# Performance work log

Measured on AMD Instinct MI355X. Metric: run time of the kernel, lower is better.

The kernel has to match this reference:

```python
import jax, jax.numpy as jnp
import numpy as np

N_NODES = 50000
N_EDGES = 800000
D_IN = 128
D_OUT = 128
NUM_RELS = 100


def setup_inputs() -> dict:
    key = jax.random.key(0)
    k1, k2, k3, k4, k5, k6, k7 = jax.random.split(key, 7)
    h = jax.random.normal(k1, (N_NODES, D_IN), dtype=jnp.float32)
    W = jax.random.normal(k2, (D_IN, D_OUT), dtype=jnp.float32) * 0.05
    attn = jax.random.normal(k3, (2 * D_OUT,), dtype=jnp.float32) * 0.05
    rel_emb = jax.random.normal(k4, (NUM_RELS, 1), dtype=jnp.float32)
    src = jax.random.randint(k5, (N_EDGES,), 0, N_NODES, dtype=jnp.int32)
    dst = jax.random.randint(k6, (N_EDGES,), 0, N_NODES, dtype=jnp.int32)
    etype = jax.random.randint(k7, (N_EDGES,), 0, NUM_RELS, dtype=jnp.int32)
    return {"h": h, "W": W, "attn": attn, "rel_emb": rel_emb,
            "src": src, "dst": dst, "etype": etype}


def reference(h, W, attn, rel_emb, src, dst, etype):
    # h: [N, d_in], W: [d_in, d_out], attn: [2*d_out], rel_emb: [R, 1]
    # src/dst/etype: [E]
    N = h.shape[0]
    d = W.shape[1]
    # padding_idx=0 in nn.Embedding -> row 0 is zero
    rel_table = rel_emb.at[0].set(0.0)
    z = h @ W  # [N, d_out]
    # attn_fc([z_src, z_dst]) = z_src @ a_l + z_dst @ a_r (split the concat-linear)
    s_src = z @ attn[:d]  # [N]
    s_dst = z @ attn[d:]  # [N]
    e = jax.nn.leaky_relu(s_src[src] + s_dst[dst])  # [E], slope 0.01 as in torch
    # segment softmax over incoming edges of each dst node
    m = jax.ops.segment_max(e, dst, num_segments=N)  # [N]
    ex = jnp.exp(e - m[dst])  # [E]
    denom = jax.ops.segment_sum(ex, dst, num_segments=N)  # [N]
    alpha = ex / denom[dst]  # [E]
    coef = rel_table[etype, 0] * alpha  # [E]  (rel_alpha * alpha)
    # weighted sum of source messages per destination node
    out = jax.ops.segment_sum(coef[:, None] * z[src], dst, num_segments=N)  # [N, d_out]
    return out
```

## Files before the change

kernel.cpp:

```cpp
#include <hip/hip_runtime.h>

#define D 128
#define GROWS 64
#define CHUNK 4096

typedef __attribute__((ext_vector_type(8))) short short8;
typedef __attribute__((ext_vector_type(4))) float float4v;

__device__ __forceinline__ ushort f2bf(float x) {
    uint u = __float_as_uint(x);
    return (ushort)((u + 0x7FFFu + ((u >> 16) & 1u)) >> 16);
}
__device__ __forceinline__ float bf_lo(uint u) { return __uint_as_float(u << 16); }
__device__ __forceinline__ float bf_hi(uint u) { return __uint_as_float(u & 0xFFFF0000u); }

__global__ __launch_bounds__(256) void convW_kernel(
    const float* __restrict__ W, ushort* __restrict__ Wtg)
{
    int idx = blockIdx.x * 256 + threadIdx.x;
    int k = idx >> 7, n = idx & 127;
    Wtg[n * 128 + k] = f2bf(W[idx]);
}

__global__ __launch_bounds__(512) void gemm_mfma_kernel(
    const float* __restrict__ h, const ushort* __restrict__ Wtg,
    const float* __restrict__ attn,
    ushort* __restrict__ zb, float* __restrict__ s_src, float* __restrict__ s_dst,
    int N)
{
    __shared__ ushort ht[GROWS * 136];
    __shared__ float psum_s[GROWS][2];
    __shared__ float psum_d[GROWS][2];
    const int tid = threadIdx.x;
    const int base = blockIdx.x * GROWS;

#pragma unroll
    for (int it = 0; it < 4; ++it) {
        int idx = it * 512 + tid;
        int r = idx >> 5, c4 = (idx & 31) * 4;
        float4 v = make_float4(0.f, 0.f, 0.f, 0.f);
        if (base + r < N) v = *(const float4*)&h[(size_t)(base + r) * D + c4];
        ushort4 u = make_ushort4(f2bf(v.x), f2bf(v.y), f2bf(v.z), f2bf(v.w));
        *(ushort4*)&ht[r * 136 + c4] = u;
    }
    __syncthreads();

    const int lane = tid & 63;
    const int wave = tid >> 6;
    const int wr = wave >> 1;
    const int wc = wave & 1;
    const int col = lane & 15;
    const int quad = lane >> 4;
    const int wm = wr * 16;

    float4v acc[4];
#pragma unroll
    for (int nt = 0; nt < 4; ++nt) acc[nt] = (float4v)(0.f);

#pragma unroll 1
    for (int kc = 0; kc < 128; kc += 32) {
        short8 a = *(const short8*)&ht[(wm + col) * 136 + kc + quad * 8];
#pragma unroll
        for (int nt = 0; nt < 4; ++nt) {
            short8 b = *(const short8*)&Wtg[(wc * 64 + nt * 16 + col) * 128 + kc + quad * 8];
            acc[nt] = __builtin_amdgcn_mfma_f32_16x16x32_bf16(a, b, acc[nt], 0, 0, 0);
        }
    }
    __syncthreads();

    float ps[4] = {0.f, 0.f, 0.f, 0.f}, pd[4] = {0.f, 0.f, 0.f, 0.f};
#pragma unroll
    for (int nt = 0; nt < 4; ++nt) {
        float aL = attn[wc * 64 + nt * 16 + col];
        float aR = attn[D + wc * 64 + nt * 16 + col];
#pragma unroll
        for (int reg = 0; reg < 4; ++reg) {
            float v = acc[nt][reg];
            ps[reg] = fmaf(v, aL, ps[reg]);
            pd[reg] = fmaf(v, aR, pd[reg]);
            ht[(wm + quad * 4 + reg) * 136 + wc * 64 + nt * 16 + col] = f2bf(v);
        }
    }
#pragma unroll
    for (int reg = 0; reg < 4; ++reg) {
#pragma unroll
        for (int off = 1; off < 16; off <<= 1) {
            ps[reg] += __shfl_xor(ps[reg], off);
            pd[reg] += __shfl_xor(pd[reg], off);
        }
        if (col == 0) {
            int rl = wm + quad * 4 + reg;
            psum_s[rl][wc] = ps[reg];
            psum_d[rl][wc] = pd[reg];
        }
    }
    __syncthreads();

    if (tid < GROWS && base + tid < N) {
        s_src[base + tid] = psum_s[tid][0] + psum_s[tid][1];
        s_dst[base + tid] = psum_d[tid][0] + psum_d[tid][1];
    }

#pragma unroll
    for (int it = 0; it < 2; ++it) {
        int idx = it * 512 + tid;
        int r = idx >> 4, c8 = idx & 15;
        if (base + r < N)
            *(uint4*)&zb[(size_t)(base + r) * D + c8 * 8] = *(uint4*)&ht[r * 136 + c8 * 8];
    }
}


__global__ __launch_bounds__(256) void binA_kernel(
    const int* __restrict__ dst, int* __restrict__ histm, int nhi, int E)
{
    __shared__ int hist[256];
    const int tid = threadIdx.x;
    hist[tid] = 0;
    __syncthreads();
    const int base = blockIdx.x * CHUNK;
#pragma unroll
    for (int it = 0; it < CHUNK / 256; ++it) {
        int i = base + it * 256 + tid;
        if (i < E) atomicAdd(&hist[dst[i] >> 8], 1);
    }
    __syncthreads();
    if (tid < nhi) histm[blockIdx.x * nhi + tid] = hist[tid];
}

__global__ __launch_bounds__(64) void binB1_kernel(
    int* __restrict__ histm, int* __restrict__ colsum, int nhi, int nchunk)
{
    const int b = blockIdx.x;
    const int t = threadIdx.x;
    const int K = (nchunk + 63) / 64;
    int v[8];
    int s = 0;
#pragma unroll
    for (int j = 0; j < 8; ++j) {
        int c = t * K + j;
        v[j] = (j < K && c < nchunk) ? histm[c * nhi + b] : 0;
        s += v[j];
    }
    int incl = s;
#pragma unroll
    for (int off = 1; off < 64; off <<= 1) {
        int u = __shfl_up(incl, off);
        if (t >= off) incl += u;
    }
    int run = incl - s;
#pragma unroll
    for (int j = 0; j < 8; ++j) {
        int c = t * K + j;
        if (j < K && c < nchunk) { histm[c * nhi + b] = run; run += v[j]; }
    }
    if (t == 63) colsum[b] = incl;
}

__global__ __launch_bounds__(256) void binB2_kernel(
    const int* __restrict__ colsum, int* __restrict__ bin_base, int nhi, int E)
{
    __shared__ int sc[256];
    const int t = threadIdx.x;
    int total = (t < nhi) ? colsum[t] : 0;
    sc[t] = total;
    __syncthreads();
    for (int off = 1; off < 256; off <<= 1) {
        int u = (t >= off) ? sc[t - off] : 0;
        __syncthreads();
        sc[t] += u;
        __syncthreads();
    }
    if (t < nhi) bin_base[t] = sc[t] - total;
    if (t == nhi - 1) bin_base[nhi] = sc[t];
}

__global__ __launch_bounds__(256) void binC_kernel(
    const int* __restrict__ src, const int* __restrict__ dst,
    const int* __restrict__ etype, const int* __restrict__ histm,
    const int* __restrict__ bin_base, uint* __restrict__ binned, int nhi, int E)
{
    __shared__ int cursor[256];
    const int tid = threadIdx.x;
    if (tid < nhi) cursor[tid] = bin_base[tid] + histm[blockIdx.x * nhi + tid];
    __syncthreads();
    const int base = blockIdx.x * CHUNK;
#pragma unroll
    for (int it = 0; it < CHUNK / 256; ++it) {
        int i = base + it * 256 + tid;
        if (i < E) {
            int d = dst[i];
            int pos = atomicAdd(&cursor[d >> 8], 1);
            binned[pos] = (uint)src[i] | ((uint)etype[i] << 16) | ((uint)(d & 255) << 23);
        }
    }
}

__global__ __launch_bounds__(256) void binD_kernel(
    const uint* __restrict__ binned, const int* __restrict__ bin_base,
    int* __restrict__ offsets, uint* __restrict__ csr, int N, int E)
{
    __shared__ int hist[256];
    __shared__ int cursor[256];
    const int t = threadIdx.x;
    const int hi = blockIdx.x;
    const int bb = bin_base[hi];
    const int be = bin_base[hi + 1];
    hist[t] = 0;
    __syncthreads();
    for (int i = bb + t; i < be; i += 256)
        atomicAdd(&hist[(binned[i] >> 23) & 0xFF], 1);
    __syncthreads();
    int total = hist[t];
    cursor[t] = total;
    __syncthreads();
    for (int off = 1; off < 256; off <<= 1) {
        int u = (t >= off) ? cursor[t - off] : 0;
        __syncthreads();
        cursor[t] += u;
        __syncthreads();
    }
    int excl = cursor[t] - total;
    int node = hi * 256 + t;
    if (node < N) offsets[node] = bb + excl;
    if (node == N - 1 || (hi == gridDim.x - 1 && t == 255)) offsets[N] = E;
    __syncthreads();
    cursor[t] = bb + excl;
    __syncthreads();
    for (int i = bb + t; i < be; i += 256) {
        uint pk = binned[i];
        int pos = atomicAdd(&cursor[(pk >> 23) & 0xFF], 1);
        csr[pos] = pk;
    }
}

__global__ __launch_bounds__(256) void aggregate_kernel(
    const uint* __restrict__ zb32, const float* __restrict__ s_src,
    const float* __restrict__ s_dst, const int* __restrict__ offsets,
    const uint* __restrict__ csr_packed, const float* __restrict__ rel_emb,
    float* __restrict__ out, int N, int R)
{
    __shared__ float rel_l[128];
    const int tid = threadIdx.x;
    if (tid < R) rel_l[tid] = (tid == 0) ? 0.f : rel_emb[tid];
    __syncthreads();

    const int lane = tid & 63;
    const int half = lane & 31;
    const int hsel = lane >> 5;
    const int d = blockIdx.x * 4 + (tid >> 6);
    if (d >= N) return;

    const int start = offsets[d];
    const int end = offsets[d + 1];
    const float sdst = s_dst[d];

    float m = -INFINITY, l = 0.f;
    float4 acc = make_float4(0.f, 0.f, 0.f, 0.f);

    for (int base = start; base < end; base += 64) {
        const int idx = base + lane;
        const bool valid = idx < end;
        const uint packed = valid ? csr_packed[idx] : 0;
        const int srcv = (int)(packed & 0xFFFF);
        const int et = (int)((packed >> 16) & 0x7F);
        float ev = -INFINITY;
        if (valid) {
            float x = s_src[srcv] + sdst;
            ev = (x > 0.f) ? x : 0.01f * x;
        }
        float cm = ev;
#pragma unroll
        for (int off = 32; off; off >>= 1) cm = fmaxf(cm, __shfl_xor(cm, off));
        const float newm = fmaxf(m, cm);
        const float scale = __expf(m - newm);
        const float p = valid ? __expf(ev - newm) : 0.f;
        float ssum = p;
#pragma unroll
        for (int off = 32; off; off >>= 1) ssum += __shfl_xor(ssum, off);
        l = l * scale + ssum;
        acc.x *= scale; acc.y *= scale; acc.z *= scale; acc.w *= scale;
        m = newm;

        const float w = p * rel_l[et];
        const int nv = min(64, end - base);
        for (int j = 0; j < nv; j += 4) {
            const int e0 = j + hsel, e1 = j + 2 + hsel;
            const float w0 = __shfl(w, e0);
            const float w1 = __shfl(w, e1);
            const int s0 = __shfl(srcv, e0);
            const int s1 = __shfl(srcv, e1);
            const uint2 u0 = *(const uint2*)(zb32 + (size_t)s0 * 64 + half * 2);
            const uint2 u1 = *(const uint2*)(zb32 + (size_t)s1 * 64 + half * 2);
            acc.x = fmaf(w0, bf_lo(u0.x), acc.x);
            acc.y = fmaf(w0, bf_hi(u0.x), acc.y);
            acc.z = fmaf(w0, bf_lo(u0.y), acc.z);
            acc.w = fmaf(w0, bf_hi(u0.y), acc.w);
            acc.x = fmaf(w1, bf_lo(u1.x), acc.x);
            acc.y = fmaf(w1, bf_hi(u1.x), acc.y);
            acc.z = fmaf(w1, bf_lo(u1.y), acc.z);
            acc.w = fmaf(w1, bf_hi(u1.y), acc.w);
        }
    }

    acc.x += __shfl_xor(acc.x, 32);
    acc.y += __shfl_xor(acc.y, 32);
    acc.z += __shfl_xor(acc.z, 32);
    acc.w += __shfl_xor(acc.w, 32);

    const float inv = (l > 0.f) ? 1.0f / l : 0.f;
    if (lane < 32) {
        float4 res = make_float4(acc.x * inv, acc.y * inv, acc.z * inv, acc.w * inv);
        *(float4*)(out + (size_t)d * D + 4 * half) = res;
    }
}

extern "C" void kernel_launch(void* const* d_in, const int* in_sizes, int n_in,
                              void* d_out, int out_size, void* d_ws, size_t ws_size,
                              hipStream_t stream)
{
    const float* h    = (const float*)d_in[0];
    const float* W    = (const float*)d_in[1];
    const float* attn = (const float*)d_in[2];
    const float* rel  = (const float*)d_in[3];
    const int*   src  = (const int*)d_in[4];
    const int*   dst  = (const int*)d_in[5];
    const int*   et   = (const int*)d_in[6];
    float* out = (float*)d_out;

    const int N = in_sizes[0] / D;
    const int E = in_sizes[4];
    const int R = in_sizes[3];

    char* p = (char*)d_ws;
    auto alloc = [&](size_t bytes) {
        char* q = p;
        p += (bytes + 255) & ~(size_t)255;
        return q;
    };
    const int nhi    = (N + 255) / 256;
    const int nchunk = (E + CHUNK - 1) / CHUNK;

    ushort* zb      = (ushort*)alloc((size_t)N * D * sizeof(ushort));
    ushort* Wtg     = (ushort*)alloc((size_t)D * D * sizeof(ushort));
    float* ssrc     = (float*)alloc((size_t)N * sizeof(float));
    float* sdst     = (float*)alloc((size_t)N * sizeof(float));
    int*   offsets  = (int*)alloc((size_t)(N + 1) * sizeof(int));
    uint*  binned   = (uint*)alloc((size_t)E * sizeof(uint));
    uint*  csr      = (uint*)alloc((size_t)E * sizeof(uint));
    int*   histm    = (int*)alloc((size_t)nchunk * nhi * sizeof(int));
    int*   colsum   = (int*)alloc((size_t)nhi * sizeof(int));
    int*   bin_base = (int*)alloc((size_t)(nhi + 1) * sizeof(int));

    const int gblocks = (N + GROWS - 1) / GROWS;

    convW_kernel<<<64, 256, 0, stream>>>(W, Wtg);
    gemm_mfma_kernel<<<gblocks, 512, 0, stream>>>(h, Wtg, attn, zb, ssrc, sdst, N);
    binA_kernel<<<nchunk, 256, 0, stream>>>(dst, histm, nhi, E);
    binB1_kernel<<<nhi, 64, 0, stream>>>(histm, colsum, nhi, nchunk);
    binB2_kernel<<<1, 256, 0, stream>>>(colsum, bin_base, nhi, E);
    binC_kernel<<<nchunk, 256, 0, stream>>>(src, dst, et, histm, bin_base, binned, nhi, E);
    binD_kernel<<<nhi, 256, 0, stream>>>(binned, bin_base, offsets, csr, N, E);
    aggregate_kernel<<<(N + 3) / 4, 256, 0, stream>>>((const uint*)zb, ssrc, sdst,
                                                      offsets, csr, rel, out, N, R);
}
```

Before: 179.4 us.

## Fuse five CSR binning kernels into one cooperative kernel with grid syncs

```diff
diff --git a/kernel.cpp b/kernel.cpp
--- a/kernel.cpp
+++ b/kernel.cpp
@@ -1,8 +1,11 @@
 #include <hip/hip_runtime.h>
+#include <hip/hip_cooperative_groups.h>
+
+namespace cg = cooperative_groups;
 
 #define D 128
 #define GROWS 64
-#define CHUNK 4096
+#define SCHUNKS 256
 
 typedef __attribute__((ext_vector_type(8))) short short8;
 typedef __attribute__((ext_vector_type(4))) float float4v;
@@ -110,127 +113,103 @@
     }
 }
 
-
-__global__ __launch_bounds__(256) void binA_kernel(
-    const int* __restrict__ dst, int* __restrict__ histm, int nhi, int E)
-{
-    __shared__ int hist[256];
+__global__ __launch_bounds__(256) void coop_sort_kernel(
+    const int* __restrict__ src, const int* __restrict__ dst,
+    const int* __restrict__ etype,
+    int* __restrict__ histm,
+    int* __restrict__ colsum, int* __restrict__ bin_base,
+    uint* __restrict__ binned, int* __restrict__ offsets, uint* __restrict__ csr,
+    int nhi, int N, int E)
+{
+    cg::grid_group grid = cg::this_grid();
+    __shared__ int sA[256];
+    __shared__ int sB[256];
     const int tid = threadIdx.x;
-    hist[tid] = 0;
-    __syncthreads();
-    const int base = blockIdx.x * CHUNK;
-#pragma unroll
-    for (int it = 0; it < CHUNK / 256; ++it) {
-        int i = base + it * 256 + tid;
-        if (i < E) atomicAdd(&hist[dst[i] >> 8], 1);
-    }
-    __syncthreads();
-    if (tid < nhi) histm[blockIdx.x * nhi + tid] = hist[tid];
-}
-
-__global__ __launch_bounds__(64) void binB1_kernel(
-    int* __restrict__ histm, int* __restrict__ colsum, int nhi, int nchunk)
-{
-    const int b = blockIdx.x;
-    const int t = threadIdx.x;
-    const int K = (nchunk + 63) / 64;
-    int v[8];
-    int s = 0;
-#pragma unroll
-    for (int j = 0; j < 8; ++j) {
-        int c = t * K + j;
-        v[j] = (j < K && c < nchunk) ? histm[c * nhi + b] : 0;
-        s += v[j];
-    }
-    int incl = s;
-#pragma unroll
-    for (int off = 1; off < 64; off <<= 1) {
-        int u = __shfl_up(incl, off);
-        if (t >= off) incl += u;
-    }
-    int run = incl - s;
-#pragma unroll
-    for (int j = 0; j < 8; ++j) {
-        int c = t * K + j;
-        if (j < K && c < nchunk) { histm[c * nhi + b] = run; run += v[j]; }
-    }
-    if (t == 63) colsum[b] = incl;
-}
-
-__global__ __launch_bounds__(256) void binB2_kernel(
-    const int* __restrict__ colsum, int* __restrict__ bin_base, int nhi, int E)
-{
-    __shared__ int sc[256];
-    const int t = threadIdx.x;
-    int total = (t < nhi) ? colsum[t] : 0;
-    sc[t] = total;
-    __syncthreads();
-    for (int off = 1; off < 256; off <<= 1) {
-        int u = (t >= off) ? sc[t - off] : 0;
-        __syncthreads();
-        sc[t] += u;
-        __syncthreads();
-    }
-    if (t < nhi) bin_base[t] = sc[t] - total;
-    if (t == nhi - 1) bin_base[nhi] = sc[t];
-}
-
-__global__ __launch_bounds__(256) void binC_kernel(
-    const int* __restrict__ src, const int* __restrict__ dst,
-    const int* __restrict__ etype, const int* __restrict__ histm,
-    const int* __restrict__ bin_base, uint* __restrict__ binned, int nhi, int E)
-{
-    __shared__ int cursor[256];
-    const int tid = threadIdx.x;
-    if (tid < nhi) cursor[tid] = bin_base[tid] + histm[blockIdx.x * nhi + tid];
-    __syncthreads();
-    const int base = blockIdx.x * CHUNK;
-#pragma unroll
-    for (int it = 0; it < CHUNK / 256; ++it) {
-        int i = base + it * 256 + tid;
-        if (i < E) {
-            int d = dst[i];
-            int pos = atomicAdd(&cursor[d >> 8], 1);
-            binned[pos] = (uint)src[i] | ((uint)etype[i] << 16) | ((uint)(d & 255) << 23);
-        }
-    }
-}
-
-__global__ __launch_bounds__(256) void binD_kernel(
-    const uint* __restrict__ binned, const int* __restrict__ bin_base,
-    int* __restrict__ offsets, uint* __restrict__ csr, int N, int E)
-{
-    __shared__ int hist[256];
-    __shared__ int cursor[256];
-    const int t = threadIdx.x;
-    const int hi = blockIdx.x;
-    const int bb = bin_base[hi];
-    const int be = bin_base[hi + 1];
-    hist[t] = 0;
-    __syncthreads();
-    for (int i = bb + t; i < be; i += 256)
-        atomicAdd(&hist[(binned[i] >> 23) & 0xFF], 1);
-    __syncthreads();
-    int total = hist[t];
-    cursor[t] = total;
-    __syncthreads();
-    for (int off = 1; off < 256; off <<= 1) {
-        int u = (t >= off) ? cursor[t - off] : 0;
-        __syncthreads();
-        cursor[t] += u;
-        __syncthreads();
-    }
-    int excl = cursor[t] - total;
-    int node = hi * 256 + t;
-    if (node < N) offsets[node] = bb + excl;
-    if (node == N - 1 || (hi == gridDim.x - 1 && t == 255)) offsets[N] = E;
-    __syncthreads();
-    cursor[t] = bb + excl;
-    __syncthreads();
-    for (int i = bb + t; i < be; i += 256) {
-        uint pk = binned[i];
-        int pos = atomicAdd(&cursor[(pk >> 23) & 0xFF], 1);
-        csr[pos] = pk;
+    const int blk = blockIdx.x;
+    const int cpb = (E + SCHUNKS - 1) / SCHUNKS;
+    const int cstart = blk * cpb;
+    const int cend = min(cstart + cpb, E);
+
+    sA[tid] = 0;
+    __syncthreads();
+    for (int i = cstart + tid; i < cend; i += 256)
+        atomicAdd(&sA[dst[i] >> 8], 1);
+    __syncthreads();
+    if (tid < nhi) histm[blk * nhi + tid] = sA[tid];
+
+    grid.sync();
+
+    if (blk < nhi) {
+        int v = histm[tid * nhi + blk];
+        sB[tid] = v;
+        __syncthreads();
+        for (int off = 1; off < 256; off <<= 1) {
+            int u = (tid >= off) ? sB[tid - off] : 0;
+            __syncthreads();
+            sB[tid] += u;
+            __syncthreads();
+        }
+        histm[tid * nhi + blk] = sB[tid] - v;
+        if (tid == 255) colsum[blk] = sB[255];
+    }
+
+    grid.sync();
+
+    if (blk == 0) {
+        int total = (tid < nhi) ? colsum[tid] : 0;
+        sB[tid] = total;
+        __syncthreads();
+        for (int off = 1; off < 256; off <<= 1) {
+            int u = (tid >= off) ? sB[tid - off] : 0;
+            __syncthreads();
+            sB[tid] += u;
+            __syncthreads();
+        }
+        if (tid < nhi) bin_base[tid] = sB[tid] - total;
+        if (tid == nhi - 1) bin_base[nhi] = sB[tid];
+    }
+
+    grid.sync();
+
+    if (tid < nhi) sB[tid] = bin_base[tid] + histm[blk * nhi + tid];
+    __syncthreads();
+    for (int i = cstart + tid; i < cend; i += 256) {
+        int d = dst[i];
+        int pos = atomicAdd(&sB[d >> 8], 1);
+        binned[pos] = (uint)src[i] | ((uint)etype[i] << 16) | ((uint)(d & 255) << 23);
+    }
+
+    grid.sync();
+
+    if (blk < nhi) {
+        const int bb = bin_base[blk];
+        const int be = bin_base[blk + 1];
+        sA[tid] = 0;
+        __syncthreads();
+        for (int i = bb + tid; i < be; i += 256)
+            atomicAdd(&sA[(binned[i] >> 23) & 0xFF], 1);
+        __syncthreads();
+        int total = sA[tid];
+        sB[tid] = total;
+        __syncthreads();
+        for (int off = 1; off < 256; off <<= 1) {
+            int u = (tid >= off) ? sB[tid - off] : 0;
+            __syncthreads();
+            sB[tid] += u;
+            __syncthreads();
+        }
+        int excl = sB[tid] - total;
+        int node = blk * 256 + tid;
+        if (node < N) offsets[node] = bb + excl;
+        if (node == N - 1) offsets[N] = E;
+        __syncthreads();
+        sB[tid] = bb + excl;
+        __syncthreads();
+        for (int i = bb + tid; i < be; i += 256) {
+            uint pk = binned[i];
+            int pos = atomicAdd(&sB[(pk >> 23) & 0xFF], 1);
+            csr[pos] = pk;
+        }
     }
 }
 
@@ -328,9 +307,9 @@
     const int*   et   = (const int*)d_in[6];
     float* out = (float*)d_out;
 
-    const int N = in_sizes[0] / D;
-    const int E = in_sizes[4];
-    const int R = in_sizes[3];
+    int N = in_sizes[0] / D;
+    int E = in_sizes[4];
+    int R = in_sizes[3];
 
     char* p = (char*)d_ws;
     auto alloc = [&](size_t bytes) {
@@ -338,8 +317,7 @@
         p += (bytes + 255) & ~(size_t)255;
         return q;
     };
-    const int nhi    = (N + 255) / 256;
-    const int nchunk = (E + CHUNK - 1) / CHUNK;
+    int nhi = (N + 255) / 256;
 
     ushort* zb      = (ushort*)alloc((size_t)N * D * sizeof(ushort));
     ushort* Wtg     = (ushort*)alloc((size_t)D * D * sizeof(ushort));
@@ -348,7 +326,7 @@
     int*   offsets  = (int*)alloc((size_t)(N + 1) * sizeof(int));
     uint*  binned   = (uint*)alloc((size_t)E * sizeof(uint));
     uint*  csr      = (uint*)alloc((size_t)E * sizeof(uint));
-    int*   histm    = (int*)alloc((size_t)nchunk * nhi * sizeof(int));
+    int*   histm    = (int*)alloc((size_t)SCHUNKS * nhi * sizeof(int));
     int*   colsum   = (int*)alloc((size_t)nhi * sizeof(int));
     int*   bin_base = (int*)alloc((size_t)(nhi + 1) * sizeof(int));
 
@@ -356,11 +334,17 @@
 
     convW_kernel<<<64, 256, 0, stream>>>(W, Wtg);
     gemm_mfma_kernel<<<gblocks, 512, 0, stream>>>(h, Wtg, attn, zb, ssrc, sdst, N);
-    binA_kernel<<<nchunk, 256, 0, stream>>>(dst, histm, nhi, E);
-    binB1_kernel<<<nhi, 64, 0, stream>>>(histm, colsum, nhi, nchunk);
-    binB2_kernel<<<1, 256, 0, stream>>>(colsum, bin_base, nhi, E);
-    binC_kernel<<<nchunk, 256, 0, stream>>>(src, dst, et, histm, bin_base, binned, nhi, E);
-    binD_kernel<<<nhi, 256, 0, stream>>>(binned, bin_base, offsets, csr, N, E);
+
+    const int* src_a = src; const int* dst_a = dst; const int* et_a = et;
+    void* sort_args[] = {
+        (void*)&src_a, (void*)&dst_a, (void*)&et_a,
+        (void*)&histm, (void*)&colsum, (void*)&bin_base,
+        (void*)&binned, (void*)&offsets, (void*)&csr,
+        (void*)&nhi, (void*)&N, (void*)&E
+    };
+    hipLaunchCooperativeKernel((void*)coop_sort_kernel, dim3(SCHUNKS), dim3(256),
+                               sort_args, 0, stream);
+
     aggregate_kernel<<<(N + 3) / 4, 256, 0, stream>>>((const uint*)zb, ssrc, sdst,
                                                       offsets, csr, rel, out, N, R);
 }
```

Result: slower. 310.3 us (+73.0%).

## Fuse dst histogram into GEMM, fold bin-base scan into binning kernels

Applied to the files above, without the earlier changes.

```diff
diff --git a/kernel.cpp b/kernel.cpp
--- a/kernel.cpp
+++ b/kernel.cpp
@@ -2,7 +2,6 @@
 
 #define D 128
 #define GROWS 64
-#define CHUNK 4096
 
 typedef __attribute__((ext_vector_type(8))) short short8;
 typedef __attribute__((ext_vector_type(4))) float float4v;
@@ -24,13 +23,14 @@
 
 __global__ __launch_bounds__(512) void gemm_mfma_kernel(
     const float* __restrict__ h, const ushort* __restrict__ Wtg,
-    const float* __restrict__ attn,
+    const float* __restrict__ attn, const int* __restrict__ dst,
     ushort* __restrict__ zb, float* __restrict__ s_src, float* __restrict__ s_dst,
-    int N)
+    int* __restrict__ histm, int nhi, int N, int E, int nblocks)
 {
     __shared__ ushort ht[GROWS * 136];
     __shared__ float psum_s[GROWS][2];
     __shared__ float psum_d[GROWS][2];
+    __shared__ int histA[256];
     const int tid = threadIdx.x;
     const int base = blockIdx.x * GROWS;
 
@@ -43,6 +43,7 @@
         ushort4 u = make_ushort4(f2bf(v.x), f2bf(v.y), f2bf(v.z), f2bf(v.w));
         *(ushort4*)&ht[r * 136 + c4] = u;
     }
+    if (tid < 256) histA[tid] = 0;
     __syncthreads();
 
     const int lane = tid & 63;
@@ -108,24 +109,14 @@
         if (base + r < N)
             *(uint4*)&zb[(size_t)(base + r) * D + c8 * 8] = *(uint4*)&ht[r * 136 + c8 * 8];
     }
-}
-
-
-__global__ __launch_bounds__(256) void binA_kernel(
-    const int* __restrict__ dst, int* __restrict__ histm, int nhi, int E)
-{
-    __shared__ int hist[256];
-    const int tid = threadIdx.x;
-    hist[tid] = 0;
-    __syncthreads();
-    const int base = blockIdx.x * CHUNK;
-#pragma unroll
-    for (int it = 0; it < CHUNK / 256; ++it) {
-        int i = base + it * 256 + tid;
-        if (i < E) atomicAdd(&hist[dst[i] >> 8], 1);
-    }
-    __syncthreads();
-    if (tid < nhi) histm[blockIdx.x * nhi + tid] = hist[tid];
+
+    const int cpb = (E + nblocks - 1) / nblocks;
+    const int cs = blockIdx.x * cpb;
+    const int ce = min(cs + cpb, E);
+    for (int i = cs + tid; i < ce; i += 512)
+        atomicAdd(&histA[dst[i] >> 8], 1);
+    __syncthreads();
+    if (tid < nhi) histm[blockIdx.x * nhi + tid] = histA[tid];
 }
 
 __global__ __launch_bounds__(64) void binB1_kernel(
@@ -134,10 +125,10 @@
     const int b = blockIdx.x;
     const int t = threadIdx.x;
     const int K = (nchunk + 63) / 64;
-    int v[8];
+    int v[16];
     int s = 0;
 #pragma unroll
-    for (int j = 0; j < 8; ++j) {
+    for (int j = 0; j < 16; ++j) {
         int c = t * K + j;
         v[j] = (j < K && c < nchunk) ? histm[c * nhi + b] : 0;
         s += v[j];
@@ -150,86 +141,87 @@
     }
     int run = incl - s;
 #pragma unroll
-    for (int j = 0; j < 8; ++j) {
+    for (int j = 0; j < 16; ++j) {
         int c = t * K + j;
         if (j < K && c < nchunk) { histm[c * nhi + b] = run; run += v[j]; }
     }
     if (t == 63) colsum[b] = incl;
-}
-
-__global__ __launch_bounds__(256) void binB2_kernel(
-    const int* __restrict__ colsum, int* __restrict__ bin_base, int nhi, int E)
-{
-    __shared__ int sc[256];
-    const int t = threadIdx.x;
-    int total = (t < nhi) ? colsum[t] : 0;
-    sc[t] = total;
-    __syncthreads();
-    for (int off = 1; off < 256; off <<= 1) {
-        int u = (t >= off) ? sc[t - off] : 0;
-        __syncthreads();
-        sc[t] += u;
-        __syncthreads();
-    }
-    if (t < nhi) bin_base[t] = sc[t] - total;
-    if (t == nhi - 1) bin_base[nhi] = sc[t];
 }
 
 __global__ __launch_bounds__(256) void binC_kernel(
     const int* __restrict__ src, const int* __restrict__ dst,
     const int* __restrict__ etype, const int* __restrict__ histm,
-    const int* __restrict__ bin_base, uint* __restrict__ binned, int nhi, int E)
-{
-    __shared__ int cursor[256];
+    const int* __restrict__ colsum, uint* __restrict__ binned,
+    int nhi, int E, int nchunk)
+{
+    __shared__ int sc[256];
+    __shared__ int cur[256];
     const int tid = threadIdx.x;
-    if (tid < nhi) cursor[tid] = bin_base[tid] + histm[blockIdx.x * nhi + tid];
-    __syncthreads();
-    const int base = blockIdx.x * CHUNK;
-#pragma unroll
-    for (int it = 0; it < CHUNK / 256; ++it) {
-        int i = base + it * 256 + tid;
-        if (i < E) {
-            int d = dst[i];
-            int pos = atomicAdd(&cursor[d >> 8], 1);
-            binned[pos] = (uint)src[i] | ((uint)etype[i] << 16) | ((uint)(d & 255) << 23);
-        }
+    int tot = (tid < nhi) ? colsum[tid] : 0;
+    sc[tid] = tot;
+    __syncthreads();
+    for (int off = 1; off < 256; off <<= 1) {
+        int u = (tid >= off) ? sc[tid - off] : 0;
+        __syncthreads();
+        sc[tid] += u;
+        __syncthreads();
+    }
+    if (tid < nhi) cur[tid] = (sc[tid] - tot) + histm[blockIdx.x * nhi + tid];
+    __syncthreads();
+    const int cpb = (E + nchunk - 1) / nchunk;
+    const int cs = blockIdx.x * cpb;
+    const int ce = min(cs + cpb, E);
+    for (int i = cs + tid; i < ce; i += 256) {
+        int d = dst[i];
+        int pos = atomicAdd(&cur[d >> 8], 1);
+        binned[pos] = (uint)src[i] | ((uint)etype[i] << 16) | ((uint)(d & 255) << 23);
     }
 }
 
 __global__ __launch_bounds__(256) void binD_kernel(
-    const uint* __restrict__ binned, const int* __restrict__ bin_base,
-    int* __restrict__ offsets, uint* __restrict__ csr, int N, int E)
-{
+    const uint* __restrict__ binned, const int* __restrict__ colsum,
+    int* __restrict__ offsets, uint* __restrict__ csr, int nhi, int N, int E)
+{
+    __shared__ int sc[256];
     __shared__ int hist[256];
-    __shared__ int cursor[256];
+    __shared__ int cur[256];
     const int t = threadIdx.x;
     const int hi = blockIdx.x;
-    const int bb = bin_base[hi];
-    const int be = bin_base[hi + 1];
+    int tot = (t < nhi) ? colsum[t] : 0;
+    sc[t] = tot;
+    __syncthreads();
+    for (int off = 1; off < 256; off <<= 1) {
+        int u = (t >= off) ? sc[t - off] : 0;
+        __syncthreads();
+        sc[t] += u;
+        __syncthreads();
+    }
+    const int bb = (hi == 0) ? 0 : sc[hi - 1];
+    const int be = sc[hi];
     hist[t] = 0;
     __syncthreads();
     for (int i = bb + t; i < be; i += 256)
         atomicAdd(&hist[(binned[i] >> 23) & 0xFF], 1);
     __syncthreads();
     int total = hist[t];
-    cursor[t] = total;
+    cur[t] = total;
     __syncthreads();
     for (int off = 1; off < 256; off <<= 1) {
-        int u = (t >= off) ? cursor[t - off] : 0;
-        __syncthreads();
-        cursor[t] += u;
-        __syncthreads();
-    }
-    int excl = cursor[t] - total;
+        int u = (t >= off) ? cur[t - off] : 0;
+        __syncthreads();
+        cur[t] += u;
+        __syncthreads();
+    }
+    int excl = cur[t] - total;
     int node = hi * 256 + t;
     if (node < N) offsets[node] = bb + excl;
-    if (node == N - 1 || (hi == gridDim.x - 1 && t == 255)) offsets[N] = E;
-    __syncthreads();
-    cursor[t] = bb + excl;
+    if (node == N - 1) offsets[N] = E;
+    __syncthreads();
+    cur[t] = bb + excl;
     __syncthreads();
     for (int i = bb + t; i < be; i += 256) {
         uint pk = binned[i];
-        int pos = atomicAdd(&cursor[(pk >> 23) & 0xFF], 1);
+        int pos = atomicAdd(&cur[(pk >> 23) & 0xFF], 1);
         csr[pos] = pk;
     }
 }
@@ -284,14 +276,16 @@
 
         const float w = p * rel_l[et];
         const int nv = min(64, end - base);
-        for (int j = 0; j < nv; j += 4) {
-            const int e0 = j + hsel, e1 = j + 2 + hsel;
-            const float w0 = __shfl(w, e0);
-            const float w1 = __shfl(w, e1);
-            const int s0 = __shfl(srcv, e0);
-            const int s1 = __shfl(srcv, e1);
+        for (int j = 0; j < nv; j += 8) {
+            const int e0 = j + hsel, e1 = j + 2 + hsel, e2 = j + 4 + hsel, e3 = j + 6 + hsel;
+            const float w0 = __shfl(w, e0), w1 = __shfl(w, e1);
+            const float w2 = __shfl(w, e2), w3 = __shfl(w, e3);
+            const int s0 = __shfl(srcv, e0), s1 = __shfl(srcv, e1);
+            const int s2 = __shfl(srcv, e2), s3 = __shfl(srcv, e3);
             const uint2 u0 = *(const uint2*)(zb32 + (size_t)s0 * 64 + half * 2);
             const uint2 u1 = *(const uint2*)(zb32 + (size_t)s1 * 64 + half * 2);
+            const uint2 u2 = *(const uint2*)(zb32 + (size_t)s2 * 64 + half * 2);
+            const uint2 u3 = *(const uint2*)(zb32 + (size_t)s3 * 64 + half * 2);
             acc.x = fmaf(w0, bf_lo(u0.x), acc.x);
             acc.y = fmaf(w0, bf_hi(u0.x), acc.y);
             acc.z = fmaf(w0, bf_lo(u0.y), acc.z);
@@ -300,6 +294,14 @@
             acc.y = fmaf(w1, bf_hi(u1.x), acc.y);
             acc.z = fmaf(w1, bf_lo(u1.y), acc.z);
             acc.w = fmaf(w1, bf_hi(u1.y), acc.w);
+            acc.x = fmaf(w2, bf_lo(u2.x), acc.x);
+            acc.y = fmaf(w2, bf_hi(u2.x), acc.y);
+            acc.z = fmaf(w2, bf_lo(u2.y), acc.z);
+            acc.w = fmaf(w2, bf_hi(u2.y), acc.w);
+            acc.x = fmaf(w3, bf_lo(u3.x), acc.x);
+            acc.y = fmaf(w3, bf_hi(u3.x), acc.y);
+            acc.z = fmaf(w3, bf_lo(u3.y), acc.z);
+            acc.w = fmaf(w3, bf_hi(u3.y), acc.w);
         }
     }
 
@@ -338,29 +340,26 @@
         p += (bytes + 255) & ~(size_t)255;
         return q;
     };
-    const int nhi    = (N + 255) / 256;
-    const int nchunk = (E + CHUNK - 1) / CHUNK;
-
-    ushort* zb      = (ushort*)alloc((size_t)N * D * sizeof(ushort));
-    ushort* Wtg     = (ushort*)alloc((size_t)D * D * sizeof(ushort));
-    float* ssrc     = (float*)alloc((size_t)N * sizeof(float));
-    float* sdst     = (float*)alloc((size_t)N * sizeof(float));
-    int*   offsets  = (int*)alloc((size_t)(N + 1) * sizeof(int));
-    uint*  binned   = (uint*)alloc((size_t)E * sizeof(uint));
-    uint*  csr      = (uint*)alloc((size_t)E * sizeof(uint));
-    int*   histm    = (int*)alloc((size_t)nchunk * nhi * sizeof(int));
-    int*   colsum   = (int*)alloc((size_t)nhi * sizeof(int));
-    int*   bin_base = (int*)alloc((size_t)(nhi + 1) * sizeof(int));
-
+    const int nhi     = (N + 255) / 256;
     const int gblocks = (N + GROWS - 1) / GROWS;
 
+    ushort* zb     = (ushort*)alloc((size_t)N * D * sizeof(ushort));
+    ushort* Wtg    = (ushort*)alloc((size_t)D * D * sizeof(ushort));
+    float* ssrc    = (float*)alloc((size_t)N * sizeof(float));
+    float* sdst    = (float*)alloc((size_t)N * sizeof(float));
+    int*   offsets = (int*)alloc((size_t)(N + 1) * sizeof(int));
+    uint*  binned  = (uint*)alloc((size_t)E * sizeof(uint));
+    uint*  csr     = (uint*)alloc((size_t)E * sizeof(uint));
+    int*   histm   = (int*)alloc((size_t)gblocks * nhi * sizeof(int));
+    int*   colsum  = (int*)alloc((size_t)nhi * sizeof(int));
+
     convW_kernel<<<64, 256, 0, stream>>>(W, Wtg);
-    gemm_mfma_kernel<<<gblocks, 512, 0, stream>>>(h, Wtg, attn, zb, ssrc, sdst, N);
-    binA_kernel<<<nchunk, 256, 0, stream>>>(dst, histm, nhi, E);
-    binB1_kernel<<<nhi, 64, 0, stream>>>(histm, colsum, nhi, nchunk);
-    binB2_kernel<<<1, 256, 0, stream>>>(colsum, bin_base, nhi, E);
-    binC_kernel<<<nchunk, 256, 0, stream>>>(src, dst, et, histm, bin_base, binned, nhi, E);
-    binD_kernel<<<nhi, 256, 0, stream>>>(binned, bin_base, offsets, csr, N, E);
+    gemm_mfma_kernel<<<gblocks, 512, 0, stream>>>(h, Wtg, attn, dst, zb, ssrc, sdst,
+                                                  histm, nhi, N, E, gblocks);
+    binB1_kernel<<<nhi, 64, 0, stream>>>(histm, colsum, nhi, gblocks);
+    binC_kernel<<<gblocks, 256, 0, stream>>>(src, dst, et, histm, colsum, binned,
+                                             nhi, E, gblocks);
+    binD_kernel<<<nhi, 256, 0, stream>>>(binned, colsum, offsets, csr, nhi, N, E);
     aggregate_kernel<<<(N + 3) / 4, 256, 0, stream>>>((const uint*)zb, ssrc, sdst,
                                                       offsets, csr, rel, out, N, R);
 }
```

Measured after the change: 172.2 us. 1.04x faster.
